# Performance work log

Hardware: AMD Instinct MI355X
Metric: run time of the kernel (lower is better)

## Reference

```python
import jax, jax.numpy as jnp
import numpy as np

IGNORE_INDEX = -100
BETA = 0.1


def setup_inputs() -> dict:
    key = jax.random.key(0)
    k0, k1, k2, k3, k4 = jax.random.split(key, 5)
    B, T, H, V = 8, 512, 2048, 32000
    x = jax.random.normal(k0, (B, T, H), jnp.float32) * 0.02
    ref_x = jax.random.normal(k1, (B, T, H), jnp.float32) * 0.02
    y = jax.random.randint(k2, (B, T), 0, V)
    W = jax.random.normal(k3, (V, H), jnp.float32) * 0.02      # policy lm_head weight
    ref_W = jax.random.normal(k4, (V, H), jnp.float32) * 0.02  # frozen reference lm_head weight
    return {"x": x, "ref_x": ref_x, "y": y, "W": W, "ref_W": ref_W}


def _batch_logps(logits, labels):
    # logits: (B, T, V), labels: (B, T). Average per-token logp over non-ignored tokens.
    mask = labels != IGNORE_INDEX
    safe = jnp.where(mask, labels, 0)
    logp = jax.nn.log_softmax(logits, axis=-1)
    tok = jnp.take_along_axis(logp, safe[..., None], axis=-1)[..., 0]  # (B, T)
    return (tok * mask).sum(-1) / mask.sum(-1)  # (B,)


def reference(x, ref_x, y, W, ref_W):
    B = x.shape[0]
    half = B // 2  # first half chosen, second half rejected

    # Policy: hidden -> vocab GEMM, then sequence-averaged log-probs of labels.
    logits = jnp.einsum("bth,vh->btv", x, W).astype(jnp.float32)
    logps = _batch_logps(logits, y)
    policy_chosen_logps, policy_rejected_logps = logps[:half], logps[half:]

    # Reference model (no grad in the original -> stop_gradient here).
    ref_logits = jnp.einsum(
        "bth,vh->btv", jax.lax.stop_gradient(ref_x), jax.lax.stop_gradient(ref_W)
    ).astype(jnp.float32)
    ref_logps = _batch_logps(ref_logits, y)
    ref_chosen_logps, ref_rejected_logps = ref_logps[:half], ref_logps[half:]

    # KTO loss (kl term is zeros in this implementation).
    chosen_logratios = policy_chosen_logps - ref_chosen_logps
    rejected_logratios = policy_rejected_logps - ref_rejected_logps
    chosen_losses = 1.0 - jax.nn.sigmoid(BETA * chosen_logratios)
    rejected_losses = 1.0 - jax.nn.sigmoid(-BETA * rejected_logratios)
    losses = jnp.concatenate([chosen_losses, rejected_losses], axis=0)
    return losses.mean()
```

## Files before the change

kernel.cpp:

```cpp
#include <hip/hip_runtime.h>
#include <hip/hip_bf16.h>

#define IGNORE_INDEX (-100)
#define BETA 0.1f

typedef __bf16 bf16x8 __attribute__((ext_vector_type(8)));
typedef float  f32x4  __attribute__((ext_vector_type(4)));

__device__ __forceinline__ void gload_lds16(const void* g, void* l) {
  __builtin_amdgcn_global_load_lds((const __attribute__((address_space(1))) void*)g,
                                   (__attribute__((address_space(3))) void*)l, 16, 0, 0);
}

__device__ __forceinline__ unsigned short f2bf(float f) {
  __hip_bfloat16 h = __float2bfloat16(f);
  return __builtin_bit_cast(unsigned short, h);
}

#define PH_BARRIER()  __builtin_amdgcn_s_barrier()
#define LGKM0()       asm volatile("s_waitcnt lgkmcnt(0)" ::: "memory")
#define VMCNT(N)      asm volatile("s_waitcnt vmcnt(" #N ")" ::: "memory")
#define SCHED_FENCE() __builtin_amdgcn_sched_barrier(0)

__global__ void cast_f32_bf16_k(const float* __restrict__ src,
                                unsigned short* __restrict__ dst, long long n) {
  long long i = (long long)blockIdx.x * blockDim.x + threadIdx.x;
  long long b = i * 8;
  if (b + 8 > n) return;
  const float4* s4 = (const float4*)(src + b);
  float4 a = s4[0], c = s4[1];
  uint4 o;
  o.x = (unsigned)f2bf(a.x) | ((unsigned)f2bf(a.y) << 16);
  o.y = (unsigned)f2bf(a.z) | ((unsigned)f2bf(a.w) << 16);
  o.z = (unsigned)f2bf(c.x) | ((unsigned)f2bf(c.y) << 16);
  o.w = (unsigned)f2bf(c.z) | ((unsigned)f2bf(c.w) << 16);
  *(uint4*)(dst + b) = o;
}


template<int MB>
__device__ __forceinline__ void ld_a(bf16x8 (&af)[4][2], const char* base,
                                     int aoff0, int aoff1) {
#pragma unroll
  for (int m = 0; m < 4; m++) {
    af[m][0] = *(const bf16x8*)(base + aoff0 + (MB + m) * 2048);
    af[m][1] = *(const bf16x8*)(base + aoff1 + (MB + m) * 2048);
  }
}

__device__ __forceinline__ void ld_b(bf16x8 (&bfr)[4][2], const char* base,
                                     int boff0, int boff1) {
#pragma unroll
  for (int n = 0; n < 4; n++) {
    bfr[n][0] = *(const bf16x8*)(base + boff0 + n * 2048);
    bfr[n][1] = *(const bf16x8*)(base + boff1 + n * 2048);
  }
}

template<int MB, int NH>
__device__ __forceinline__ void mfma_quad(f32x4 (&acc)[8][4], bf16x8 (&af)[4][2],
                                          bf16x8 (&bfr)[4][2]) {
#pragma unroll
  for (int m = 0; m < 4; m++)
#pragma unroll
    for (int n = 0; n < 2; n++)
#pragma unroll
      for (int k = 0; k < 2; k++)
        acc[MB + m][NH * 2 + n] = __builtin_amdgcn_mfma_f32_16x16x32_bf16(
            af[m][k], bfr[NH * 2 + n][k], acc[MB + m][NH * 2 + n], 0, 0, 0);
}

__device__ __forceinline__ void stage2(const unsigned short* s, char* d) {
  gload_lds16(s, d);
  gload_lds16(s + 16384, d + 1024);
}

__global__ __launch_bounds__(512, 2) void gemm_lse(
    const unsigned short* __restrict__ A,
    const unsigned short* __restrict__ B,
    const int* __restrict__ labels,
    float2* __restrict__ partials,
    float* __restrict__ label_logit) {
  int bid = blockIdx.x;
  int swz = (bid & 7) * 250 + (bid >> 3);
  const int m0 = (swz & 15) * 256;
  const int vtile = swz >> 4;
  const int n0 = vtile * 256;

  const int tid = threadIdx.x;
  const int lane = tid & 63;
  const int w = tid >> 6;
  const int wm = w >> 2, wn = w & 3;
  const int quad = lane >> 4, r16 = lane & 15;

  __shared__ char smem[131072] __attribute__((aligned(128)));
  char* smemc = smem;
  char* buf0 = smemc;
  char* buf1 = smemc + 65536;

  const int csw = ((lane & 7) ^ (lane >> 3)) * 8;
  const unsigned short* Ag = A + (size_t)(m0 + w * 16 + (lane >> 3)) * 2048 + csw;
  const unsigned short* Bg = B + (size_t)(n0 + w * 16 + (lane >> 3)) * 2048 + csw;
  char* dstA = smemc + w * 2048 + lane * 16;
  char* dstB = dstA + 32768;

  const int s7 = r16 & 7;
  const int c0 = ((quad ^ s7) << 4);
  const int c1 = (((4 | quad) ^ s7) << 4);
  const int aoff0 = wm * 16384 + r16 * 128 + c0;
  const int aoff1 = wm * 16384 + r16 * 128 + c1;
  const int brow = (wn & 1) * 64 + r16;
  const int boff0 = 32768 + (wn >> 1) * 16384 + brow * 128 + c0;
  const int boff1 = 32768 + (wn >> 1) * 16384 + brow * 128 + c1;

  bf16x8 af[4][2], bfr[4][2];
  f32x4 acc[8][4] = {};

  stage2(Bg,                dstB);
  stage2(Bg + 262144,       dstB + 16384);
  stage2(Ag,                dstA);
  stage2(Ag + 262144,       dstA + 16384);
  stage2(Bg + 64,           dstB + 65536);
  stage2(Bg + 262144 + 64,  dstB + 65536 + 16384);
  stage2(Ag + 64,           dstA + 65536);
  VMCNT(6);
  PH_BARRIER();

#pragma unroll 1
  for (int i = 0; i < 16; ++i) {
    const int kt1 = 2 * i + 1, kt2 = 2 * i + 2, kt3 = 2 * i + 3;
    const bool full = (i < 15);

    ld_a<0>(af, buf0, aoff0, aoff1);
    ld_b(bfr, buf0, boff0, boff1);
    stage2(Ag + 262144 + (size_t)kt1 * 64, dstA + 65536 + 16384);
    SCHED_FENCE(); PH_BARRIER(); LGKM0();
    __builtin_amdgcn_s_setprio(1); mfma_quad<0, 0>(acc, af, bfr);
    __builtin_amdgcn_s_setprio(0); SCHED_FENCE(); PH_BARRIER();
    if (full) stage2(Bg + (size_t)kt2 * 64, dstB);
    SCHED_FENCE(); PH_BARRIER();
    __builtin_amdgcn_s_setprio(1); mfma_quad<0, 1>(acc, af, bfr);
    __builtin_amdgcn_s_setprio(0); SCHED_FENCE(); PH_BARRIER();
    ld_a<4>(af, buf0, aoff0, aoff1);
    if (full) stage2(Bg + 262144 + (size_t)kt2 * 64, dstB + 16384);
    SCHED_FENCE(); PH_BARRIER(); LGKM0();
    __builtin_amdgcn_s_setprio(1); mfma_quad<4, 0>(acc, af, bfr);
    __builtin_amdgcn_s_setprio(0); SCHED_FENCE(); PH_BARRIER();
    if (full) { stage2(Ag + (size_t)kt2 * 64, dstA); VMCNT(6); }
    else      { VMCNT(0); }
    SCHED_FENCE(); PH_BARRIER();
    __builtin_amdgcn_s_setprio(1); mfma_quad<4, 1>(acc, af, bfr);
    __builtin_amdgcn_s_setprio(0); SCHED_FENCE(); PH_BARRIER();

    ld_a<0>(af, buf1, aoff0, aoff1);
    ld_b(bfr, buf1, boff0, boff1);
    if (full) stage2(Ag + 262144 + (size_t)kt2 * 64, dstA + 16384);
    SCHED_FENCE(); PH_BARRIER(); LGKM0();
    __builtin_amdgcn_s_setprio(1); mfma_quad<0, 0>(acc, af, bfr);
    __builtin_amdgcn_s_setprio(0); SCHED_FENCE(); PH_BARRIER();
    if (full) stage2(Bg + (size_t)kt3 * 64, dstB + 65536);
    SCHED_FENCE(); PH_BARRIER();
    __builtin_amdgcn_s_setprio(1); mfma_quad<0, 1>(acc, af, bfr);
    __builtin_amdgcn_s_setprio(0); SCHED_FENCE(); PH_BARRIER();
    ld_a<4>(af, buf1, aoff0, aoff1);
    if (full) stage2(Bg + 262144 + (size_t)kt3 * 64, dstB + 65536 + 16384);
    SCHED_FENCE(); PH_BARRIER(); LGKM0();
    __builtin_amdgcn_s_setprio(1); mfma_quad<4, 0>(acc, af, bfr);
    __builtin_amdgcn_s_setprio(0); SCHED_FENCE(); PH_BARRIER();
    if (full) { stage2(Ag + (size_t)kt3 * 64, dstA + 65536); VMCNT(6); }
    SCHED_FENCE(); PH_BARRIER();
    __builtin_amdgcn_s_setprio(1); mfma_quad<4, 1>(acc, af, bfr);
    __builtin_amdgcn_s_setprio(0); SCHED_FENCE(); PH_BARRIER();
  }

  __syncthreads();
  float2* red = (float2*)smemc;
  int* lbl = (int*)(smemc + 8192);
  if (tid < 256) lbl[tid] = labels[m0 + tid];

#pragma unroll
  for (int mi = 0; mi < 8; mi++) {
#pragma unroll
    for (int e = 0; e < 4; e++) {
      float v0 = acc[mi][0][e], v1 = acc[mi][1][e], v2 = acc[mi][2][e], v3 = acc[mi][3][e];
      float mx = fmaxf(fmaxf(v0, v1), fmaxf(v2, v3));
#pragma unroll
      for (int d = 1; d < 16; d <<= 1) mx = fmaxf(mx, __shfl_xor(mx, d));
      float s = expf(v0 - mx) + expf(v1 - mx) + expf(v2 - mx) + expf(v3 - mx);
#pragma unroll
      for (int d = 1; d < 16; d <<= 1) s += __shfl_xor(s, d);
      if (r16 == 0) {
        int row = wm * 128 + mi * 16 + quad * 4 + e;
        red[wn * 256 + row] = make_float2(mx, s);
      }
    }
  }
  __syncthreads();

#pragma unroll
  for (int mi = 0; mi < 8; mi++) {
#pragma unroll
    for (int e = 0; e < 4; e++) {
      int row = wm * 128 + mi * 16 + quad * 4 + e;
      int lb = lbl[row];
#pragma unroll
      for (int ni = 0; ni < 4; ni++) {
        int col = n0 + wn * 64 + ni * 16 + r16;
        if (lb == col) label_logit[m0 + row] = acc[mi][ni][e];
      }
    }
  }
  if (tid < 256) {
    float2 p0 = red[tid], p1 = red[256 + tid], p2 = red[512 + tid], p3 = red[768 + tid];
    float M = fmaxf(fmaxf(p0.x, p1.x), fmaxf(p2.x, p3.x));
    float S = p0.y * expf(p0.x - M) + p1.y * expf(p1.x - M) +
              p2.y * expf(p2.x - M) + p3.y * expf(p3.x - M);
    partials[(size_t)(m0 + tid) * 125 + vtile] = make_float2(M, S);
  }
}

__global__ void row_lp_k(const float2* __restrict__ parts,
                         const float* __restrict__ lablog,
                         float* __restrict__ rowlp) {
  int row = blockIdx.x * 4 + (threadIdx.x >> 6);
  int lane = threadIdx.x & 63;
  const float2* P = parts + (size_t)row * 125;
  float m = -1e30f, s = 0.f;
  for (int j = lane; j < 125; j += 64) {
    float2 p = P[j];
    if (p.x > m) { s = s * expf(m - p.x) + p.y; m = p.x; }
    else          s += p.y * expf(p.x - m);
  }
#pragma unroll
  for (int d = 1; d < 64; d <<= 1) {
    float om = __shfl_xor(m, d);
    float os = __shfl_xor(s, d);
    float M = fmaxf(m, om);
    s = s * expf(m - M) + os * expf(om - M);
    m = M;
  }
  if (lane == 0) rowlp[row] = lablog[row] - (m + logf(s));
}

__global__ void reduce_batch_k(const float* __restrict__ rowlp,
                               const int* __restrict__ labels,
                               float* __restrict__ blp) {
  int path = blockIdx.x >> 3, batch = blockIdx.x & 7;
  int t = threadIdx.x;
  int lab = labels[batch * 512 + t];
  float v = rowlp[path * 4096 + batch * 512 + t];
  bool ok = (lab != IGNORE_INDEX);
  float sum = ok ? v : 0.f;
  float cnt = ok ? 1.f : 0.f;
#pragma unroll
  for (int d = 1; d < 64; d <<= 1) { sum += __shfl_xor(sum, d); cnt += __shfl_xor(cnt, d); }
  __shared__ float ws_[8], wc_[8];
  if ((t & 63) == 0) { ws_[t >> 6] = sum; wc_[t >> 6] = cnt; }
  __syncthreads();
  if (t == 0) {
    float S = 0.f, C = 0.f;
    for (int k = 0; k < 8; k++) { S += ws_[k]; C += wc_[k]; }
    blp[blockIdx.x] = (C > 0.f) ? S / C : 0.f;
  }
}

__global__ void final_loss(const float* __restrict__ batch_lp, float* __restrict__ out) {
  if (threadIdx.x == 0 && blockIdx.x == 0) {
    float tot = 0.f;
    for (int b = 0; b < 8; b++) {
      float d = batch_lp[b] - batch_lp[8 + b];
      float z = (b < 4) ? (BETA * d) : (-BETA * d);
      float sg = 1.f / (1.f + expf(-z));
      tot += 1.f - sg;
    }
    out[0] = tot / 8.f;
  }
}

extern "C" void kernel_launch(void* const* d_in, const int* in_sizes, int n_in,
                              void* d_out, int out_size, void* d_ws, size_t ws_size,
                              hipStream_t stream) {
  const float* x     = (const float*)d_in[0];
  const float* ref_x = (const float*)d_in[1];
  const int*   y     = (const int*)d_in[2];
  const float* W     = (const float*)d_in[3];
  const float* ref_W = (const float*)d_in[4];

  unsigned short* xb  = (unsigned short*)d_ws;
  unsigned short* rxb = xb + (size_t)8388608;
  unsigned short* Wb  = rxb + (size_t)8388608;
  char* p2 = (char*)(Wb + (size_t)65536000);
  float2* parts = (float2*)p2;
  float* lablog = (float*)(p2 + (size_t)8192000);
  float* rowlp  = lablog + 8192;
  float* blp    = rowlp + 8192;

  cast_f32_bf16_k<<<4096, 256, 0, stream>>>(x, xb, 8388608LL);
  cast_f32_bf16_k<<<4096, 256, 0, stream>>>(ref_x, rxb, 8388608LL);

  cast_f32_bf16_k<<<32000, 256, 0, stream>>>(W, Wb, 65536000LL);
  gemm_lse<<<2000, 512, 0, stream>>>(xb, Wb, y, parts, lablog);

  cast_f32_bf16_k<<<32000, 256, 0, stream>>>(ref_W, Wb, 65536000LL);
  gemm_lse<<<2000, 512, 0, stream>>>(rxb, Wb, y, parts + (size_t)4096 * 125, lablog + 4096);

  row_lp_k<<<2048, 256, 0, stream>>>(parts, lablog, rowlp);
  reduce_batch_k<<<16, 512, 0, stream>>>(rowlp, y, blp);
  final_loss<<<1, 64, 0, stream>>>(blp, (float*)d_out);
}
```

Baseline: 1.648 ms.

## Switch GEMM inner loop to 32x32x16 MFMA with a transposed LDS layout

```diff
diff --git a/kernel.cpp b/kernel.cpp
--- a/kernel.cpp
+++ b/kernel.cpp
@@ -5,7 +5,7 @@
 #define BETA 0.1f
 
 typedef __bf16 bf16x8 __attribute__((ext_vector_type(8)));
-typedef float  f32x4  __attribute__((ext_vector_type(4)));
+typedef float  f32x16 __attribute__((ext_vector_type(16)));
 
 __device__ __forceinline__ void gload_lds16(const void* g, void* l) {
   __builtin_amdgcn_global_load_lds((const __attribute__((address_space(1))) void*)g,
@@ -21,6 +21,8 @@
 #define LGKM0()       asm volatile("s_waitcnt lgkmcnt(0)" ::: "memory")
 #define VMCNT(N)      asm volatile("s_waitcnt vmcnt(" #N ")" ::: "memory")
 #define SCHED_FENCE() __builtin_amdgcn_sched_barrier(0)
+#define PRIO1()       __builtin_amdgcn_s_setprio(1)
+#define PRIO0()       __builtin_amdgcn_s_setprio(0)
 
 __global__ void cast_f32_bf16_k(const float* __restrict__ src,
                                 unsigned short* __restrict__ dst, long long n) {
@@ -38,36 +40,26 @@
 }
 
 
-template<int MB>
-__device__ __forceinline__ void ld_a(bf16x8 (&af)[4][2], const char* base,
-                                     int aoff0, int aoff1) {
-#pragma unroll
-  for (int m = 0; m < 4; m++) {
-    af[m][0] = *(const bf16x8*)(base + aoff0 + (MB + m) * 2048);
-    af[m][1] = *(const bf16x8*)(base + aoff1 + (MB + m) * 2048);
-  }
-}
-
-__device__ __forceinline__ void ld_b(bf16x8 (&bfr)[4][2], const char* base,
-                                     int boff0, int boff1) {
-#pragma unroll
-  for (int n = 0; n < 4; n++) {
-    bfr[n][0] = *(const bf16x8*)(base + boff0 + n * 2048);
-    bfr[n][1] = *(const bf16x8*)(base + boff1 + n * 2048);
-  }
-}
-
-template<int MB, int NH>
-__device__ __forceinline__ void mfma_quad(f32x4 (&acc)[8][4], bf16x8 (&af)[4][2],
-                                          bf16x8 (&bfr)[4][2]) {
-#pragma unroll
-  for (int m = 0; m < 4; m++)
-#pragma unroll
-    for (int n = 0; n < 2; n++)
-#pragma unroll
-      for (int k = 0; k < 2; k++)
-        acc[MB + m][NH * 2 + n] = __builtin_amdgcn_mfma_f32_16x16x32_bf16(
-            af[m][k], bfr[NH * 2 + n][k], acc[MB + m][NH * 2 + n], 0, 0, 0);
+__device__ __forceinline__ void ld_a32(bf16x8 (&af)[4], const char* pa) {
+#pragma unroll
+  for (int ks = 0; ks < 4; ks++) af[ks] = *(const bf16x8*)(pa + ks * 256);
+}
+
+__device__ __forceinline__ void ld_b32(bf16x8 (&b)[2][4], const char* pb) {
+#pragma unroll
+  for (int nf = 0; nf < 2; nf++)
+#pragma unroll
+    for (int ks = 0; ks < 4; ks++)
+      b[nf][ks] = *(const bf16x8*)(pb + nf * 4096 + ks * 256);
+}
+
+__device__ __forceinline__ void mfma_ph(f32x16& c0, f32x16& c1,
+                                        const bf16x8 (&a)[4], const bf16x8 (&b)[2][4]) {
+#pragma unroll
+  for (int ks = 0; ks < 4; ks++) {
+    c0 = __builtin_amdgcn_mfma_f32_32x32x16_bf16(a[ks], b[0][ks], c0, 0, 0, 0);
+    c1 = __builtin_amdgcn_mfma_f32_32x32x16_bf16(a[ks], b[1][ks], c1, 0, 0, 0);
+  }
 }
 
 __device__ __forceinline__ void stage2(const unsigned short* s, char* d) {
@@ -91,86 +83,86 @@
   const int lane = tid & 63;
   const int w = tid >> 6;
   const int wm = w >> 2, wn = w & 3;
-  const int quad = lane >> 4, r16 = lane & 15;
 
   __shared__ char smem[131072] __attribute__((aligned(128)));
   char* smemc = smem;
-  char* buf0 = smemc;
-  char* buf1 = smemc + 65536;
-
-  const int csw = ((lane & 7) ^ (lane >> 3)) * 8;
-  const unsigned short* Ag = A + (size_t)(m0 + w * 16 + (lane >> 3)) * 2048 + csw;
-  const unsigned short* Bg = B + (size_t)(n0 + w * 16 + (lane >> 3)) * 2048 + csw;
-  char* dstA = smemc + w * 2048 + lane * 16;
-  char* dstB = dstA + 32768;
-
-  const int s7 = r16 & 7;
-  const int c0 = ((quad ^ s7) << 4);
-  const int c1 = (((4 | quad) ^ s7) << 4);
-  const int aoff0 = wm * 16384 + r16 * 128 + c0;
-  const int aoff1 = wm * 16384 + r16 * 128 + c1;
-  const int brow = (wn & 1) * 64 + r16;
-  const int boff0 = 32768 + (wn >> 1) * 16384 + brow * 128 + c0;
-  const int boff1 = 32768 + (wn >> 1) * 16384 + brow * 128 + c1;
-
-  bf16x8 af[4][2], bfr[4][2];
-  f32x4 acc[8][4] = {};
-
-  stage2(Bg,                dstB);
-  stage2(Bg + 262144,       dstB + 16384);
-  stage2(Ag,                dstA);
-  stage2(Ag + 262144,       dstA + 16384);
-  stage2(Bg + 64,           dstB + 65536);
-  stage2(Bg + 262144 + 64,  dstB + 65536 + 16384);
-  stage2(Ag + 64,           dstA + 65536);
+
+  const int lane7 = lane & 7, laneC = lane >> 3;
+  const unsigned short* Ag = A + (size_t)(m0 + w * 16 + lane7) * 2048 + laneC * 8;
+  const unsigned short* Bg = B + (size_t)(n0 + w * 16 + lane7) * 2048 + laneC * 8;
+  char* dA = smemc + w * 2048 + lane * 16;
+  char* dB = dA + 32768;
+
+  const int laneterm = ((lane >> 3) & 3) * 1024 + (lane >> 5) * 128 + (lane & 7) * 16;
+  const char* pA0 = smemc + wm * 16384 + laneterm;
+  const char* pB0 = smemc + 32768 + wn * 8192 + laneterm;
+  const char* pA1 = pA0 + 65536;
+  const char* pB1 = pB0 + 65536;
+
+  bf16x8 bfr[2][4], af0[4], af1[4], af2[4], af3[4];
+  f32x16 acc[4][2] = {};
+
+  stage2(Bg,                 dB);
+  stage2(Bg + 262144,        dB + 16384);
+  stage2(Ag,                 dA);
+  stage2(Ag + 262144,        dA + 16384);
+  stage2(Bg + 64,            dB + 65536);
+  stage2(Bg + 262144 + 64,   dB + 65536 + 16384);
+  stage2(Ag + 64,            dA + 65536);
   VMCNT(6);
   PH_BARRIER();
 
 #pragma unroll 1
   for (int i = 0; i < 16; ++i) {
-    const int kt1 = 2 * i + 1, kt2 = 2 * i + 2, kt3 = 2 * i + 3;
+    const size_t kt1 = (size_t)(2 * i + 1) * 64;
+    const size_t kt2 = (size_t)(2 * i + 2) * 64;
+    const size_t kt3 = (size_t)(2 * i + 3) * 64;
     const bool full = (i < 15);
 
-    ld_a<0>(af, buf0, aoff0, aoff1);
-    ld_b(bfr, buf0, boff0, boff1);
-    stage2(Ag + 262144 + (size_t)kt1 * 64, dstA + 65536 + 16384);
-    SCHED_FENCE(); PH_BARRIER(); LGKM0();
-    __builtin_amdgcn_s_setprio(1); mfma_quad<0, 0>(acc, af, bfr);
-    __builtin_amdgcn_s_setprio(0); SCHED_FENCE(); PH_BARRIER();
-    if (full) stage2(Bg + (size_t)kt2 * 64, dstB);
-    SCHED_FENCE(); PH_BARRIER();
-    __builtin_amdgcn_s_setprio(1); mfma_quad<0, 1>(acc, af, bfr);
-    __builtin_amdgcn_s_setprio(0); SCHED_FENCE(); PH_BARRIER();
-    ld_a<4>(af, buf0, aoff0, aoff1);
-    if (full) stage2(Bg + 262144 + (size_t)kt2 * 64, dstB + 16384);
-    SCHED_FENCE(); PH_BARRIER(); LGKM0();
-    __builtin_amdgcn_s_setprio(1); mfma_quad<4, 0>(acc, af, bfr);
-    __builtin_amdgcn_s_setprio(0); SCHED_FENCE(); PH_BARRIER();
-    if (full) { stage2(Ag + (size_t)kt2 * 64, dstA); VMCNT(6); }
+    ld_b32(bfr, pB0);
+    ld_a32(af0, pA0);
+    stage2(Ag + 262144 + kt1, dA + 65536 + 16384);
+    SCHED_FENCE(); PH_BARRIER(); LGKM0();
+    PRIO1(); mfma_ph(acc[0][0], acc[0][1], af0, bfr); PRIO0();
+    SCHED_FENCE(); PH_BARRIER();
+    ld_a32(af1, pA0 + 4096);
+    if (full) stage2(Bg + kt2, dB);
+    SCHED_FENCE(); PH_BARRIER(); LGKM0();
+    PRIO1(); mfma_ph(acc[1][0], acc[1][1], af1, bfr); PRIO0();
+    SCHED_FENCE(); PH_BARRIER();
+    ld_a32(af2, pA0 + 8192);
+    ld_a32(af3, pA0 + 12288);
+    if (full) stage2(Bg + 262144 + kt2, dB + 16384);
+    SCHED_FENCE(); PH_BARRIER(); LGKM0();
+    PRIO1(); mfma_ph(acc[2][0], acc[2][1], af2, bfr); PRIO0();
+    SCHED_FENCE(); PH_BARRIER();
+    if (full) { stage2(Ag + kt2, dA); VMCNT(6); }
     else      { VMCNT(0); }
     SCHED_FENCE(); PH_BARRIER();
-    __builtin_amdgcn_s_setprio(1); mfma_quad<4, 1>(acc, af, bfr);
-    __builtin_amdgcn_s_setprio(0); SCHED_FENCE(); PH_BARRIER();
-
-    ld_a<0>(af, buf1, aoff0, aoff1);
-    ld_b(bfr, buf1, boff0, boff1);
-    if (full) stage2(Ag + 262144 + (size_t)kt2 * 64, dstA + 16384);
-    SCHED_FENCE(); PH_BARRIER(); LGKM0();
-    __builtin_amdgcn_s_setprio(1); mfma_quad<0, 0>(acc, af, bfr);
-    __builtin_amdgcn_s_setprio(0); SCHED_FENCE(); PH_BARRIER();
-    if (full) stage2(Bg + (size_t)kt3 * 64, dstB + 65536);
-    SCHED_FENCE(); PH_BARRIER();
-    __builtin_amdgcn_s_setprio(1); mfma_quad<0, 1>(acc, af, bfr);
-    __builtin_amdgcn_s_setprio(0); SCHED_FENCE(); PH_BARRIER();
-    ld_a<4>(af, buf1, aoff0, aoff1);
-    if (full) stage2(Bg + 262144 + (size_t)kt3 * 64, dstB + 65536 + 16384);
-    SCHED_FENCE(); PH_BARRIER(); LGKM0();
-    __builtin_amdgcn_s_setprio(1); mfma_quad<4, 0>(acc, af, bfr);
-    __builtin_amdgcn_s_setprio(0); SCHED_FENCE(); PH_BARRIER();
-    if (full) { stage2(Ag + (size_t)kt3 * 64, dstA + 65536); VMCNT(6); }
-    SCHED_FENCE(); PH_BARRIER();
-    __builtin_amdgcn_s_setprio(1); mfma_quad<4, 1>(acc, af, bfr);
-    __builtin_amdgcn_s_setprio(0); SCHED_FENCE(); PH_BARRIER();
+    PRIO1(); mfma_ph(acc[3][0], acc[3][1], af3, bfr); PRIO0();
+    SCHED_FENCE(); PH_BARRIER();
+
+    ld_b32(bfr, pB1);
+    ld_a32(af0, pA1);
+    if (full) stage2(Ag + 262144 + kt2, dA + 16384);
+    SCHED_FENCE(); PH_BARRIER(); LGKM0();
+    PRIO1(); mfma_ph(acc[0][0], acc[0][1], af0, bfr); PRIO0();
+    SCHED_FENCE(); PH_BARRIER();
+    ld_a32(af1, pA1 + 4096);
+    if (full) stage2(Bg + kt3, dB + 65536);
+    SCHED_FENCE(); PH_BARRIER(); LGKM0();
+    PRIO1(); mfma_ph(acc[1][0], acc[1][1], af1, bfr); PRIO0();
+    SCHED_FENCE(); PH_BARRIER();
+    ld_a32(af2, pA1 + 8192);
+    ld_a32(af3, pA1 + 12288);
+    if (full) stage2(Bg + 262144 + kt3, dB + 65536 + 16384);
+    SCHED_FENCE(); PH_BARRIER(); LGKM0();
+    PRIO1(); mfma_ph(acc[2][0], acc[2][1], af2, bfr); PRIO0();
+    SCHED_FENCE(); PH_BARRIER();
+    if (full) { stage2(Ag + kt3, dA + 65536); VMCNT(6); }
+    SCHED_FENCE(); PH_BARRIER();
+    PRIO1(); mfma_ph(acc[3][0], acc[3][1], af3, bfr); PRIO0();
+    SCHED_FENCE(); PH_BARRIER();
   }
 
   __syncthreads();
@@ -179,18 +171,18 @@
   if (tid < 256) lbl[tid] = labels[m0 + tid];
 
 #pragma unroll
-  for (int mi = 0; mi < 8; mi++) {
-#pragma unroll
-    for (int e = 0; e < 4; e++) {
-      float v0 = acc[mi][0][e], v1 = acc[mi][1][e], v2 = acc[mi][2][e], v3 = acc[mi][3][e];
-      float mx = fmaxf(fmaxf(v0, v1), fmaxf(v2, v3));
-#pragma unroll
-      for (int d = 1; d < 16; d <<= 1) mx = fmaxf(mx, __shfl_xor(mx, d));
-      float s = expf(v0 - mx) + expf(v1 - mx) + expf(v2 - mx) + expf(v3 - mx);
-#pragma unroll
-      for (int d = 1; d < 16; d <<= 1) s += __shfl_xor(s, d);
-      if (r16 == 0) {
-        int row = wm * 128 + mi * 16 + quad * 4 + e;
+  for (int mf = 0; mf < 4; mf++) {
+#pragma unroll
+    for (int reg = 0; reg < 16; reg++) {
+      float v0 = acc[mf][0][reg], v1 = acc[mf][1][reg];
+      float mx = fmaxf(v0, v1);
+#pragma unroll
+      for (int d = 1; d < 32; d <<= 1) mx = fmaxf(mx, __shfl_xor(mx, d));
+      float s = expf(v0 - mx) + expf(v1 - mx);
+#pragma unroll
+      for (int d = 1; d < 32; d <<= 1) s += __shfl_xor(s, d);
+      if ((lane & 31) == 0) {
+        int row = wm * 128 + mf * 32 + (reg & 3) + 8 * (reg >> 2) + ((lane >> 5) << 2);
         red[wn * 256 + row] = make_float2(mx, s);
       }
     }
@@ -198,15 +190,15 @@
   __syncthreads();
 
 #pragma unroll
-  for (int mi = 0; mi < 8; mi++) {
-#pragma unroll
-    for (int e = 0; e < 4; e++) {
-      int row = wm * 128 + mi * 16 + quad * 4 + e;
+  for (int mf = 0; mf < 4; mf++) {
+#pragma unroll
+    for (int reg = 0; reg < 16; reg++) {
+      int row = wm * 128 + mf * 32 + (reg & 3) + 8 * (reg >> 2) + ((lane >> 5) << 2);
       int lb = lbl[row];
 #pragma unroll
-      for (int ni = 0; ni < 4; ni++) {
-        int col = n0 + wn * 64 + ni * 16 + r16;
-        if (lb == col) label_logit[m0 + row] = acc[mi][ni][e];
+      for (int nf = 0; nf < 2; nf++) {
+        int col = n0 + wn * 64 + nf * 32 + (lane & 31);
+        if (lb == col) label_logit[m0 + row] = acc[mf][nf][reg];
       }
     }
   }
```

New measurement: 2.017 ms. +22.4%, slower.
